# Kernel optimization log

Measured on AMD Instinct MI355X. Metric: run time of the kernel, lower is better.

Reference implementation:

```python
import jax, jax.numpy as jnp
import numpy as np

K = 3  # kernel size (conv_identity_params(32, 3) -> kernel=3, pad=1)
P = 1  # padding


def _unfold(x):
    # torch.nn.Unfold(kernel_size=K, padding=P) on (N,C,H,W) -> (N, C*K*K, H*W)
    N, C, H, W = x.shape
    xp = jnp.pad(x, ((0, 0), (0, 0), (P, P), (P, P)))
    # (N, C, K*K, H, W): channel slowest, then kernel row-major -> matches torch unfold layout
    patches = jnp.stack([xp[:, :, i:i + H, j:j + W]
                         for i in range(K) for j in range(K)], axis=2)
    return patches.reshape(N, C, K * K, H * W)


def _fold(y, H, W):
    # torch.nn.Fold(kernel_size=K, output_size=(H,W), padding=P) on (N, C*K*K, H*W) -> (N,C,H,W)
    N = y.shape[0]
    C = y.shape[1] // (K * K)
    yb = y.reshape(N, C, K, K, H, W)  # torch interprets channel dim as (C, kh, kw)
    out = jnp.zeros((N, C, H + 2 * P, W + 2 * P), y.dtype)
    for i in range(K):
        for j in range(K):
            out = out.at[:, :, i:i + H, j:j + W].add(yb[:, :, i, j])
    return out[:, :, P:P + H, P:P + W]


def setup_inputs() -> dict:
    key = jax.random.key(0)
    k1, k2, k3 = jax.random.split(key, 3)
    N, C, H, W = 16, 4, 32, 32
    S = H * W
    x = jax.random.uniform(k1, (N, C, H, W), dtype=jnp.float32)
    # expanded weight: (N, N, S1*S2, C, C, K*K)
    weight = jax.random.normal(k2, (N, N, S, C, C, K * K), dtype=jnp.float32) * 0.05
    chan_map = jax.random.normal(k3, (N, N, C, C), dtype=jnp.float32) * 0.25
    mask = jnp.ones((N, N), dtype=jnp.float32)
    return {"x": x, "weight": weight, "chan_map": chan_map, "mask": mask}


def reference(x, weight, chan_map, mask):
    N, C, H, W = x.shape
    S = H * W
    # unfold -> (N, S, C, K^2)  == 'usck'
    xufld = _unfold(x).reshape(N, C, K * K, S).transpose(0, 3, 1, 2)
    # combined weight: mask over (u,v), chan_map over (u,v,c,o)  -> (u,v,s,c,o,k)
    cw = weight * mask[:, :, None, None, None, None] \
                * chan_map[:, :, None, :, :, None]
    # einsum 'uvsck, uvscok -> vsok' (x has singleton v dim in torch)
    mapped = jnp.einsum('usck,uvscok->vsok', xufld, cw)  # (N, S, C, K^2)
    # transpose(2,3) -> (N, S, K^2, C) -> reshape (N, S, K^2*C) -> (N, K^2*C, S)
    ufld = mapped.transpose(0, 1, 3, 2).reshape(N, S, K * K * C).transpose(0, 2, 1)
    return _fold(ufld, H, W)
```

## Files before the change

kernel.cpp:

```cpp
#include <hip/hip_runtime.h>

#define NB 16
#define CC 4
#define HH 32
#define WW 32
#define SS 1024

__global__ __launch_bounds__(576) void main_kernel(
    const float* __restrict__ x,
    const float* __restrict__ wgt,
    const float* __restrict__ chan_map,
    const float* __restrict__ mask,
    float* __restrict__ mapped)
{
    __shared__ __align__(16) float XT[16 * 16 * 36];
    __shared__ __align__(16) float CM[16 * 16];
    __shared__ __align__(16) float4 RED[16 * 36];
    const int v   = blockIdx.y;
    const int s0  = blockIdx.x * 16;
    const int tid = threadIdx.x;

    for (int t = tid; t < 16 * 16 * 36; t += 576) {
        int u = t / 576;
        int rem = t % 576;
        int sl = rem / 36, kc = rem % 36;
        int k = kc >> 2, c = kc & 3;
        int s = s0 + sl;
        int h = (s >> 5) + (k / 3) - 1;
        int w = (s & 31) + (k % 3) - 1;
        float val = 0.f;
        if (h >= 0 && h < HH && w >= 0 && w < WW)
            val = x[((u * CC + c) * HH + h) * WW + w];
        XT[t] = val;
    }
    if (tid < 256) {
        int u = tid >> 4, o = (tid >> 2) & 3, c = tid & 3;
        CM[tid] = chan_map[((u * 16 + v) * 4 + c) * 4 + o] * mask[u * 16 + v];
    }
    __syncthreads();

    const int sl = tid / 36;
    const int q  = tid % 36;
    const int s  = s0 + sl;

    int xt_off[4], cm_off[4];
#pragma unroll
    for (int e = 0; e < 4; ++e) {
        int r = 4 * q + e;
        int c = r / 36;
        int o = (r / 9) & 3;
        int k = r % 9;
        xt_off[e] = sl * 36 + k * 4 + c;
        cm_off[e] = o * 4 + c;
    }

    const float* wp = wgt + (size_t)v * 147456 + (size_t)s * 144 + 4 * q;
    float4 acc = make_float4(0.f, 0.f, 0.f, 0.f);
#pragma unroll 4
    for (int u = 0; u < 16; ++u) {
        float4 w4 = *(const float4*)(wp + (size_t)u * 2359296);
        acc.x += w4.x * XT[u * 576 + xt_off[0]] * CM[u * 16 + cm_off[0]];
        acc.y += w4.y * XT[u * 576 + xt_off[1]] * CM[u * 16 + cm_off[1]];
        acc.z += w4.z * XT[u * 576 + xt_off[2]] * CM[u * 16 + cm_off[2]];
        acc.w += w4.w * XT[u * 576 + xt_off[3]] * CM[u * 16 + cm_off[3]];
    }

    RED[sl * 36 + q] = acc;
    __syncthreads();
    if (q < 9) {
        float4 t0 = RED[sl * 36 + q];
        float4 t1 = RED[sl * 36 + q + 9];
        float4 t2 = RED[sl * 36 + q + 18];
        float4 t3 = RED[sl * 36 + q + 27];
        float tot[4] = { t0.x + t1.x + t2.x + t3.x,
                         t0.y + t1.y + t2.y + t3.y,
                         t0.z + t1.z + t2.z + t3.z,
                         t0.w + t1.w + t2.w + t3.w };
        float* mp = mapped + v * (SS * 36) + s * 36;
#pragma unroll
        for (int e = 0; e < 4; ++e) {
            int r = 4 * q + e;
            int o = r / 9, k = r % 9;
            mp[k * 4 + o] = tot[e];
        }
    }
}

__global__ void fold_kernel(const float* __restrict__ mapped, float* __restrict__ out) {
    int t = blockIdx.x * blockDim.x + threadIdx.x;
    if (t >= NB * CC * HH * WW) return;
    int xx = t & 31, y = (t >> 5) & 31, c = (t >> 10) & 3, v = t >> 12;
    float sum = 0.f;
#pragma unroll
    for (int i = 0; i < 3; ++i) {
        int h = y + 1 - i;
        if (h < 0 || h >= HH) continue;
#pragma unroll
        for (int j = 0; j < 3; ++j) {
            int w = xx + 1 - j;
            if (w < 0 || w >= WW) continue;
            sum += mapped[v * (SS * 36) + (h * 32 + w) * 36 + (c * 9 + i * 3 + j)];
        }
    }
    out[t] = sum;
}

extern "C" void kernel_launch(void* const* d_in, const int* in_sizes, int n_in,
                              void* d_out, int out_size, void* d_ws, size_t ws_size,
                              hipStream_t stream) {
    const float* x    = (const float*)d_in[0];
    const float* wgt  = (const float*)d_in[1];
    const float* cmap = (const float*)d_in[2];
    const float* mask = (const float*)d_in[3];
    float* out = (float*)d_out;

    float* mapped = (float*)d_ws;

    main_kernel<<<dim3(SS / 16, NB), 576, 0, stream>>>(x, wgt, cmap, mask, mapped);
    fold_kernel<<<(NB * CC * HH * WW + 255) / 256, 256, 0, stream>>>(mapped, out);
}
```

Measured before the change: 237.1 us.

## Precompute unfolded input in separate kernel and use nontemporal weight loads

Moves the im2col gather out of the main kernel into a standalone unfold kernel that writes the patches to workspace. The main kernel then loads its tile with contiguous vectorised float4 copies, and it loads the weights with nontemporal hints because they are streamed only once. This removes the redundant, scattered per-block gather of x (each block re-gathered all 16 batches). In exchange it adds an extra kernel launch, a round trip of about 2.4MB through workspace, and a larger workspace footprint.

```diff
diff --git a/kernel.cpp b/kernel.cpp
--- a/kernel.cpp
+++ b/kernel.cpp
@@ -6,8 +6,25 @@
 #define WW 32
 #define SS 1024
 
+typedef float f4 __attribute__((ext_vector_type(4)));
+
+__global__ void unfold_kernel(const float* __restrict__ x, float* __restrict__ xu) {
+    int idx = blockIdx.x * blockDim.x + threadIdx.x;
+    if (idx >= NB * SS * 36) return;
+    int c = idx & 3;
+    int k = (idx >> 2) % 9;
+    int s = (idx / 36) & (SS - 1);
+    int u = idx / (SS * 36);
+    int h = (s >> 5) + (k / 3) - 1;
+    int w = (s & 31) + (k % 3) - 1;
+    float v = 0.f;
+    if (h >= 0 && h < HH && w >= 0 && w < WW)
+        v = x[((u * CC + c) * HH + h) * WW + w];
+    xu[idx] = v;
+}
+
 __global__ __launch_bounds__(576) void main_kernel(
-    const float* __restrict__ x,
+    const float* __restrict__ xu,
     const float* __restrict__ wgt,
     const float* __restrict__ chan_map,
     const float* __restrict__ mask,
@@ -20,18 +37,15 @@
     const int s0  = blockIdx.x * 16;
     const int tid = threadIdx.x;
 
-    for (int t = tid; t < 16 * 16 * 36; t += 576) {
-        int u = t / 576;
-        int rem = t % 576;
-        int sl = rem / 36, kc = rem % 36;
-        int k = kc >> 2, c = kc & 3;
-        int s = s0 + sl;
-        int h = (s >> 5) + (k / 3) - 1;
-        int w = (s & 31) + (k % 3) - 1;
-        float val = 0.f;
-        if (h >= 0 && h < HH && w >= 0 && w < WW)
-            val = x[((u * CC + c) * HH + h) * WW + w];
-        XT[t] = val;
+    {
+        const f4* src = (const f4*)xu;
+        f4* dst = (f4*)XT;
+#pragma unroll
+        for (int i = 0; i < 4; ++i) {
+            int t = tid + i * 576;
+            int u = t / 144, r = t % 144;
+            dst[t] = src[u * 9216 + s0 * 9 + r];
+        }
     }
     if (tid < 256) {
         int u = tid >> 4, o = (tid >> 2) & 3, c = tid & 3;
@@ -55,17 +69,17 @@
     }
 
     const float* wp = wgt + (size_t)v * 147456 + (size_t)s * 144 + 4 * q;
-    float4 acc = make_float4(0.f, 0.f, 0.f, 0.f);
+    f4 acc = (f4)0.f;
 #pragma unroll 4
     for (int u = 0; u < 16; ++u) {
-        float4 w4 = *(const float4*)(wp + (size_t)u * 2359296);
+        f4 w4 = __builtin_nontemporal_load((const f4*)(wp + (size_t)u * 2359296));
         acc.x += w4.x * XT[u * 576 + xt_off[0]] * CM[u * 16 + cm_off[0]];
         acc.y += w4.y * XT[u * 576 + xt_off[1]] * CM[u * 16 + cm_off[1]];
         acc.z += w4.z * XT[u * 576 + xt_off[2]] * CM[u * 16 + cm_off[2]];
         acc.w += w4.w * XT[u * 576 + xt_off[3]] * CM[u * 16 + cm_off[3]];
     }
 
-    RED[sl * 36 + q] = acc;
+    RED[sl * 36 + q] = make_float4(acc.x, acc.y, acc.z, acc.w);
     __syncthreads();
     if (q < 9) {
         float4 t0 = RED[sl * 36 + q];
@@ -114,8 +128,10 @@
     const float* mask = (const float*)d_in[3];
     float* out = (float*)d_out;
 
-    float* mapped = (float*)d_ws;
+    float* xu     = (float*)d_ws;
+    float* mapped = xu + NB * SS * 36;
 
-    main_kernel<<<dim3(SS / 16, NB), 576, 0, stream>>>(x, wgt, cmap, mask, mapped);
+    unfold_kernel<<<(NB * SS * 36 + 255) / 256, 256, 0, stream>>>(x, xu);
+    main_kernel<<<dim3(SS / 16, NB), 576, 0, stream>>>(xu, wgt, cmap, mask, mapped);
     fold_kernel<<<(NB * CC * HH * WW + 255) / 256, 256, 0, stream>>>(mapped, out);
 }
```

Result: faster. 213.9 us (-9.8%).
